# Optimization experiments

Hardware: AMD Instinct MI355X
Metric: run time of the kernel (lower is better)

The kernel has to match this reference:

```python
import jax, jax.numpy as jnp
import numpy as np

B, T, N, C, D = 8, 12, 1024, 64, 10

def setup_inputs() -> dict:
    key = jax.random.key(0)
    ks = jax.random.split(key, 7)
    x = jax.random.normal(ks[0], (B, T, N, C), dtype=jnp.float32)
    e1 = jax.random.normal(ks[1], (N, D), dtype=jnp.float32)
    e2 = jax.random.normal(ks[2], (N, D), dtype=jnp.float32)
    # buffer: sym-normalized adjacency after the __init__-time softmax
    A_sym = jax.random.uniform(ks[3], (N, N), dtype=jnp.float32)
    weights_pool = jax.random.normal(ks[4], (N, C, C), dtype=jnp.float32) * 0.02
    bias_pool = jax.random.normal(ks[5], (N, C), dtype=jnp.float32) * 0.02
    alpha = jnp.array([0.9], dtype=jnp.float32)
    beta = jnp.array([0.9], dtype=jnp.float32)
    gamma = jnp.array([0.1], dtype=jnp.float32)
    return {"x": x, "node_embeddings1": e1, "node_embeddings2": e2,
            "A_sym": A_sym, "weights_pool": weights_pool, "bias_pool": bias_pool,
            "alpha": alpha, "beta": beta, "gamma": gamma}


def reference(x, node_embeddings1, node_embeddings2, A_sym, weights_pool,
              bias_pool, alpha, beta, gamma):
    n = node_embeddings1.shape[0]
    # dynamic supports: relu(tanh(E1 E2^T - E2 E1^T)) + I
    s = jnp.tanh(node_embeddings1 @ node_embeddings2.T
                 - node_embeddings2 @ node_embeddings1.T)
    supports = jnp.eye(n, dtype=x.dtype) + jax.nn.relu(s)          # (N,N)

    # static branch: row-softmax of the precomputed sym-norm adjacency
    A = jax.nn.softmax(A_sym, axis=-1)                              # (N,N)
    x_static = jax.nn.relu(jnp.einsum('nm,btmc->btnc', A, x))       # (B,T,N,C)

    # spatial attention branch (note: softmax over the TIME axis, as in source)
    score = jnp.einsum('btnc,btmc->btnm', x, x)                     # (B,T,N,N)
    score = jax.nn.softmax(score, axis=1)
    x_sa = jax.nn.relu(jnp.einsum('btnm,btmc->btnc', score, x))     # (B,T,N,C)

    # adaptive graph conv: per-node weights/bias from supports
    weights = jnp.einsum('nd,dio->nio', supports, weights_pool)     # (N,C,C)
    bias = supports @ bias_pool                                     # (N,C)
    x_g = jnp.einsum('nm,btmc->btnc', supports, x)                  # (B,T,N,C)
    x_gconv = jax.nn.relu(jnp.einsum('btni,nio->btno', x_g, weights) + bias)

    return alpha * x_gconv + beta * x_sa + gamma * x_static
```

## Files before the change

kernel.cpp:

```cpp
#include <hip/hip_runtime.h>
#include <math.h>

#define Bdim 8
#define Tdim 12
#define BT   96
#define Ndim 1024
#define Cdim 64
#define Ddim 10
#define Jdim 6144
#define IOdim 4096

typedef __attribute__((ext_vector_type(4))) float f32x4;
typedef __attribute__((ext_vector_type(8))) short bf16x8;
typedef __attribute__((ext_vector_type(4))) _Float16 f16x4;

__device__ inline short f2bf(float f) {
    union { float f; unsigned u; } v; v.f = f;
    return (short)((v.u + 0x8000u) >> 16);
}
__device__ inline float bf2f(short s) {
    union { float f; unsigned u; } v; v.u = ((unsigned)(unsigned short)s) << 16;
    return v.f;
}
__device__ inline void load_lds16(const void* g, void* l) {
    __builtin_amdgcn_global_load_lds(
        (const __attribute__((address_space(1))) unsigned int*)g,
        (__attribute__((address_space(3))) unsigned int*)l, 16, 0, 0);
}
__device__ inline float fexp(float x) { return __expf(x); }
__device__ inline float frcp(float x) { return __builtin_amdgcn_rcpf(x); }
__device__ inline float flog(float x) { return __logf(x); }

__global__ __launch_bounds__(256) void k_supports(
    const float* __restrict__ e1, const float* __restrict__ e2,
    short* __restrict__ Sbf)
{
    int idx = blockIdx.x * 256 + threadIdx.x;
    int i = idx >> 10, j = idx & 1023;
    float s = 0.f;
#pragma unroll
    for (int d = 0; d < Ddim; ++d)
        s += e1[i * Ddim + d] * e2[j * Ddim + d]
           - e2[i * Ddim + d] * e1[j * Ddim + d];
    float t = 1.f - 2.f * frcp(fexp(2.f * s) + 1.f);
    float v = fmaxf(t, 0.f);
    if (i == j) v += 1.f;
    Sbf[idx] = f2bf(v);
}

__global__ __launch_bounds__(256) void k_softmax_rows(
    const float* __restrict__ In, short* __restrict__ Out)
{
    int row = blockIdx.x;
    const float* r = In + (size_t)row * Ndim;
    short* o = Out + (size_t)row * Ndim;
    __shared__ float red[256];
    int tid = threadIdx.x;
    float vals[4];
    float lmax = -INFINITY;
#pragma unroll
    for (int i = 0; i < 4; ++i) { vals[i] = r[tid + 256 * i]; lmax = fmaxf(lmax, vals[i]); }
    red[tid] = lmax; __syncthreads();
    for (int s = 128; s > 0; s >>= 1) {
        if (tid < s) red[tid] = fmaxf(red[tid], red[tid + s]);
        __syncthreads();
    }
    float m = red[0]; __syncthreads();
    float lsum = 0.f;
#pragma unroll
    for (int i = 0; i < 4; ++i) { vals[i] = fexp(vals[i] - m); lsum += vals[i]; }
    red[tid] = lsum; __syncthreads();
    for (int s = 128; s > 0; s >>= 1) {
        if (tid < s) red[tid] += red[tid + s];
        __syncthreads();
    }
    float inv = frcp(red[0]);
#pragma unroll
    for (int i = 0; i < 4; ++i) o[tid + 256 * i] = f2bf(vals[i] * inv);
}

__global__ __launch_bounds__(256) void k_cvt_x(
    const float* __restrict__ x, short* __restrict__ xbf, short* __restrict__ xT)
{
    __shared__ float Lt[64][65];
    int bt = blockIdx.y, n0 = blockIdx.x * 64;
    const float* src = x + (size_t)bt * 65536 + (size_t)n0 * 64;
    int tid = threadIdx.x;
#pragma unroll
    for (int p = 0; p < 4; ++p) {
        int idx = p * 256 + tid;
        int r = idx >> 4, c4 = idx & 15;
        float4 v = *(const float4*)&src[r * 64 + c4 * 4];
        short4 s4 = make_short4(f2bf(v.x), f2bf(v.y), f2bf(v.z), f2bf(v.w));
        *(short4*)&xbf[(size_t)bt * 65536 + (size_t)(n0 + r) * 64 + c4 * 4] = s4;
        Lt[r][c4 * 4 + 0] = v.x; Lt[r][c4 * 4 + 1] = v.y;
        Lt[r][c4 * 4 + 2] = v.z; Lt[r][c4 * 4 + 3] = v.w;
    }
    __syncthreads();
#pragma unroll
    for (int p = 0; p < 4; ++p) {
        int idx = p * 256 + tid;
        int c = idx >> 4, k4 = idx & 15;
        short4 s4 = make_short4(f2bf(Lt[k4 * 4 + 0][c]), f2bf(Lt[k4 * 4 + 1][c]),
                                f2bf(Lt[k4 * 4 + 2][c]), f2bf(Lt[k4 * 4 + 3][c]));
        *(short4*)&xT[(size_t)bt * 65536 + (size_t)c * 1024 + n0 + k4 * 4] = s4;
    }
}

__global__ __launch_bounds__(256) void k_cvt_wp(
    const float* __restrict__ wp, short* __restrict__ wpT)
{
    __shared__ float Lt[64][65];
    int k0 = blockIdx.y * 64, j0 = blockIdx.x * 64;
    int tid = threadIdx.x;
#pragma unroll
    for (int p = 0; p < 4; ++p) {
        int idx = p * 256 + tid;
        int r = idx >> 4, c4 = idx & 15;
        float4 v = *(const float4*)&wp[(size_t)(k0 + r) * IOdim + j0 + c4 * 4];
        Lt[r][c4 * 4 + 0] = v.x; Lt[r][c4 * 4 + 1] = v.y;
        Lt[r][c4 * 4 + 2] = v.z; Lt[r][c4 * 4 + 3] = v.w;
    }
    __syncthreads();
#pragma unroll
    for (int p = 0; p < 4; ++p) {
        int idx = p * 256 + tid;
        int c = idx >> 4, k4 = idx & 15;
        short4 s4 = make_short4(f2bf(Lt[k4 * 4 + 0][c]), f2bf(Lt[k4 * 4 + 1][c]),
                                f2bf(Lt[k4 * 4 + 2][c]), f2bf(Lt[k4 * 4 + 3][c]));
        *(short4*)&wpT[(size_t)(j0 + c) * 1024 + k0 + k4 * 4] = s4;
    }
}

__global__ __launch_bounds__(256) void k_cvt_bp(
    const float* __restrict__ bp, short* __restrict__ bpT)
{
    __shared__ float Lt[64][65];
    int k0 = blockIdx.x * 64;
    int tid = threadIdx.x;
#pragma unroll
    for (int p = 0; p < 4; ++p) {
        int idx = p * 256 + tid;
        int r = idx >> 4, c4 = idx & 15;
        float4 v = *(const float4*)&bp[(size_t)(k0 + r) * 64 + c4 * 4];
        Lt[r][c4 * 4 + 0] = v.x; Lt[r][c4 * 4 + 1] = v.y;
        Lt[r][c4 * 4 + 2] = v.z; Lt[r][c4 * 4 + 3] = v.w;
    }
    __syncthreads();
#pragma unroll
    for (int p = 0; p < 4; ++p) {
        int idx = p * 256 + tid;
        int c = idx >> 4, k4 = idx & 15;
        short4 s4 = make_short4(f2bf(Lt[k4 * 4 + 0][c]), f2bf(Lt[k4 * 4 + 1][c]),
                                f2bf(Lt[k4 * 4 + 2][c]), f2bf(Lt[k4 * 4 + 3][c]));
        *(short4*)&bpT[(size_t)c * 1024 + k0 + k4 * 4] = s4;
    }
}

template<int MODE>
__global__ __launch_bounds__(256) void k_gemm_bt(
    const short* __restrict__ A, const short* __restrict__ Bm,
    float* __restrict__ Cf, short* __restrict__ Cb,
    const float* __restrict__ gamma_p)
{
    __shared__ short At[128 * 64];
    __shared__ short Bt[128 * 64];
    const int tid = threadIdx.x;
    const int w = tid >> 6, l = tid & 63;
    const int l15 = l & 15, q = l >> 4;
    const int n0 = blockIdx.x * 128, j0 = blockIdx.y * 128;
    const int wr = (w & 1) * 64, wc = (w >> 1) * 64;
    const int lrow = l >> 3, lc8 = l & 7;

    f32x4 acc[4][4];
#pragma unroll
    for (int i = 0; i < 4; ++i)
#pragma unroll
        for (int j = 0; j < 4; ++j) acc[i][j] = (f32x4)0.f;

    for (int k0 = 0; k0 < 1024; k0 += 64) {
        __syncthreads();
#pragma unroll
        for (int p = 0; p < 4; ++p) {
            int r = p * 32 + w * 8 + lrow;
            int sc = lc8 ^ (r & 7);
            load_lds16(A + (size_t)(n0 + r) * 1024 + k0 + sc * 8,
                       &At[(p * 32 + w * 8) * 64]);
            load_lds16(Bm + (size_t)(j0 + r) * 1024 + k0 + sc * 8,
                       &Bt[(p * 32 + w * 8) * 64]);
        }
        __syncthreads();
#pragma unroll
        for (int ks = 0; ks < 2; ++ks) {
            bf16x8 af[4], bf[4];
#pragma unroll
            for (int rt = 0; rt < 4; ++rt) {
                int row = wr + rt * 16 + l15;
                int pos = (ks * 4 + q) ^ (row & 7);
                af[rt] = *(const bf16x8*)&At[row * 64 + pos * 8];
            }
#pragma unroll
            for (int ct = 0; ct < 4; ++ct) {
                int row = wc + ct * 16 + l15;
                int pos = (ks * 4 + q) ^ (row & 7);
                bf[ct] = *(const bf16x8*)&Bt[row * 64 + pos * 8];
            }
#pragma unroll
            for (int rt = 0; rt < 4; ++rt)
#pragma unroll
                for (int ct = 0; ct < 4; ++ct)
                    acc[rt][ct] = __builtin_amdgcn_mfma_f32_16x16x32_bf16(
                        af[rt], bf[ct], acc[rt][ct], 0, 0, 0);
        }
    }

    float gmm = (MODE == 0) ? gamma_p[0] : 0.f;
#pragma unroll
    for (int rt = 0; rt < 4; ++rt) {
        int nr = n0 + wr + rt * 16 + q * 4;
#pragma unroll
        for (int ct = 0; ct < 4; ++ct) {
            int j = j0 + wc + ct * 16 + l15;
#pragma unroll
            for (int r = 0; r < 4; ++r) {
                float v = acc[rt][ct][r];
                int n = nr + r;
                if (MODE == 1) {
                    Cb[(size_t)n * IOdim + j] = f2bf(v);
                } else if (n < 1024) {
                    int bt = j >> 6, c = j & 63;
                    Cf[(size_t)bt * 65536 + (size_t)n * 64 + c] = gmm * fmaxf(v, 0.f);
                } else {
                    Cb[(size_t)(n - 1024) * Jdim + j] = f2bf(v);
                }
            }
        }
    }
}

__global__ __launch_bounds__(256, 4) void k_sa_z(
    const short* __restrict__ xbf, short* __restrict__ Lh)
{
    __shared__ short Xn[64 * 64];
    __shared__ short Xm[64 * 64];

    int id = blockIdx.x;
    int b = id & 7;
    int r = id >> 3;
    int tn = r & 15, tm = r >> 4;
    int tid = threadIdx.x;
    int w = tid >> 6, l = tid & 63;
    int l15 = l & 15, q = l >> 4;
    int lrow = l >> 3, lc8 = l & 7;
    int n0 = tn * 64, m0 = tm * 64;
    int wn = (w & 1) * 32, wm = (w >> 1) * 32;

    const short* Xb = xbf + (size_t)b * Tdim * Ndim * Cdim;
    short* Lb = Lh + ((size_t)b << 20);

    f32x4 M[2][2], Z[2][2];
#pragma unroll
    for (int nh = 0; nh < 2; ++nh)
#pragma unroll
        for (int mh = 0; mh < 2; ++mh) { M[nh][mh] = (f32x4)(-INFINITY); Z[nh][mh] = (f32x4)0.f; }

    for (int t = 0; t < Tdim; ++t) {
        const short* xt = Xb + (size_t)t * (Ndim * Cdim);
        __syncthreads();
#pragma unroll
        for (int p = 0; p < 2; ++p) {
            int rr = p * 32 + w * 8 + lrow;
            int sc = lc8 ^ (rr & 7);
            load_lds16(xt + (size_t)(n0 + rr) * 64 + sc * 8, &Xn[(p * 32 + w * 8) * 64]);
            load_lds16(xt + (size_t)(m0 + rr) * 64 + sc * 8, &Xm[(p * 32 + w * 8) * 64]);
        }
        __syncthreads();

        f32x4 sacc[2][2];
        sacc[0][0] = (f32x4)0.f; sacc[0][1] = (f32x4)0.f;
        sacc[1][0] = (f32x4)0.f; sacc[1][1] = (f32x4)0.f;
#pragma unroll
        for (int ch = 0; ch < 2; ++ch) {
            bf16x8 qb[2], af[2];
#pragma unroll
            for (int nh = 0; nh < 2; ++nh) {
                int row = wn + nh * 16 + l15;
                int pos = (ch * 4 + q) ^ (row & 7);
                qb[nh] = *(const bf16x8*)&Xn[row * 64 + pos * 8];
            }
#pragma unroll
            for (int mh = 0; mh < 2; ++mh) {
                int row = wm + mh * 16 + l15;
                int pos = (ch * 4 + q) ^ (row & 7);
                af[mh] = *(const bf16x8*)&Xm[row * 64 + pos * 8];
            }
#pragma unroll
            for (int nh = 0; nh < 2; ++nh)
#pragma unroll
                for (int mh = 0; mh < 2; ++mh)
                    sacc[nh][mh] = __builtin_amdgcn_mfma_f32_16x16x32_bf16(
                        af[mh], qb[nh], sacc[nh][mh], 0, 0, 0);
        }
#pragma unroll
        for (int nh = 0; nh < 2; ++nh)
#pragma unroll
            for (int mh = 0; mh < 2; ++mh)
#pragma unroll
                for (int i = 0; i < 4; ++i) {
                    float s  = sacc[nh][mh][i];
                    float mo = M[nh][mh][i];
                    float mn = fmaxf(mo, s);
                    Z[nh][mh][i] = Z[nh][mh][i] * fexp(mo - mn) + fexp(s - mn);
                    M[nh][mh][i] = mn;
                }
    }
#pragma unroll
    for (int nh = 0; nh < 2; ++nh)
#pragma unroll
        for (int mh = 0; mh < 2; ++mh) {
            f16x4 ev;
#pragma unroll
            for (int i = 0; i < 4; ++i)
                ev[i] = (_Float16)(M[nh][mh][i] + flog(Z[nh][mh][i]));
            *(f16x4*)&Lb[(size_t)(n0 + wn + nh * 16 + l15) * 1024
                         + m0 + wm + mh * 16 + q * 4] = ev;
        }
}

__global__ __launch_bounds__(256, 4) void k_sa_pv(
    const short* __restrict__ xbf, const short* __restrict__ xT,
    const short* __restrict__ Lh, float* __restrict__ Out,
    const float* __restrict__ beta_p)
{
    __shared__ short Xm[32 * 72];
    __shared__ short XTl[64 * 40];
    __shared__ short Pl[4][16][40];

    int id = blockIdx.x;
    int b = id & 7;
    int r = id >> 3;
    int nt = r & 7, t = r >> 3;
    int tid = threadIdx.x;
    int w = tid >> 6, l = tid & 63;
    int l15 = l & 15, q = l >> 4;
    int n0 = nt * 128 + w * 32;

    const short* Xb  = xbf + ((size_t)b * Tdim + t) * (Ndim * Cdim);
    const short* XTb = xT  + ((size_t)b * Tdim + t) * (Ndim * Cdim);
    const short* Lb  = Lh + ((size_t)b << 20);

    int srow  = tid >> 3, sc8 = tid & 7;
    int srow2 = tid >> 2, sc4 = tid & 3;

    bf16x8 qf[2][2];
#pragma unroll
    for (int nh = 0; nh < 2; ++nh)
#pragma unroll
        for (int ch = 0; ch < 2; ++ch)
            qf[nh][ch] = *(const bf16x8*)&Xb[(n0 + nh * 16 + l15) * 64 + ch * 32 + q * 8];

    f32x4 oacc[2][4];
#pragma unroll
    for (int nh = 0; nh < 2; ++nh)
#pragma unroll
        for (int ct = 0; ct < 4; ++ct) oacc[nh][ct] = (f32x4)0.f;

    bf16x8 v  = *(const bf16x8*)&Xb[(size_t)srow * 64 + sc8 * 8];
    bf16x8 v2 = *(const bf16x8*)&XTb[(size_t)srow2 * 1024 + sc4 * 8];
    f16x4 e[2][2];
#pragma unroll
    for (int nh = 0; nh < 2; ++nh)
#pragma unroll
        for (int mh = 0; mh < 2; ++mh)
            e[nh][mh] = *(const f16x4*)&Lb[(size_t)(n0 + nh * 16 + l15) * 1024
                                           + mh * 16 + q * 4];

    for (int mi = 0; mi < 32; ++mi) {
        __syncthreads();
        *(bf16x8*)&Xm[srow * 72 + sc8 * 8]   = v;
        *(bf16x8*)&XTl[srow2 * 40 + sc4 * 8] = v2;
        __syncthreads();

        int m0n = (mi < 31 ? mi + 1 : 31) * 32;
        bf16x8 vn  = *(const bf16x8*)&Xb[(size_t)(m0n + srow) * 64 + sc8 * 8];
        bf16x8 v2n = *(const bf16x8*)&XTb[(size_t)srow2 * 1024 + m0n + sc4 * 8];
        f16x4 en[2][2];
#pragma unroll
        for (int nh = 0; nh < 2; ++nh)
#pragma unroll
            for (int mh = 0; mh < 2; ++mh)
                en[nh][mh] = *(const f16x4*)&Lb[(size_t)(n0 + nh * 16 + l15) * 1024
                                                + m0n + mh * 16 + q * 4];

        f32x4 sacc[2][2];
        sacc[0][0] = (f32x4)0.f; sacc[0][1] = (f32x4)0.f;
        sacc[1][0] = (f32x4)0.f; sacc[1][1] = (f32x4)0.f;
#pragma unroll
        for (int ch = 0; ch < 2; ++ch) {
#pragma unroll
            for (int mh = 0; mh < 2; ++mh) {
                bf16x8 af = *(const bf16x8*)&Xm[(mh * 16 + l15) * 72 + ch * 32 + q * 8];
                sacc[0][mh] = __builtin_amdgcn_mfma_f32_16x16x32_bf16(
                    af, qf[0][ch], sacc[0][mh], 0, 0, 0);
                sacc[1][mh] = __builtin_amdgcn_mfma_f32_16x16x32_bf16(
                    af, qf[1][ch], sacc[1][mh], 0, 0, 0);
            }
        }
#pragma unroll
        for (int nh = 0; nh < 2; ++nh) {
#pragma unroll
            for (int mh = 0; mh < 2; ++mh) {
                f32x4 p = sacc[nh][mh];
                f16x4 ee = e[nh][mh];
                unsigned u0 = (unsigned)(unsigned short)f2bf(fexp(p[0] - (float)ee[0]))
                            | ((unsigned)(unsigned short)f2bf(fexp(p[1] - (float)ee[1])) << 16);
                unsigned u1 = (unsigned)(unsigned short)f2bf(fexp(p[2] - (float)ee[2]))
                            | ((unsigned)(unsigned short)f2bf(fexp(p[3] - (float)ee[3])) << 16);
                *(uint2*)&Pl[w][l15][mh * 16 + q * 4] = make_uint2(u0, u1);
            }
            bf16x8 pf = *(const bf16x8*)&Pl[w][l15][q * 8];
#pragma unroll
            for (int ct = 0; ct < 4; ++ct) {
                bf16x8 bfr = *(const bf16x8*)&XTl[(ct * 16 + l15) * 40 + q * 8];
                oacc[nh][ct] = __builtin_amdgcn_mfma_f32_16x16x32_bf16(
                    pf, bfr, oacc[nh][ct], 0, 0, 0);
            }
        }
        v = vn; v2 = v2n;
#pragma unroll
        for (int nh = 0; nh < 2; ++nh)
#pragma unroll
            for (int mh = 0; mh < 2; ++mh) e[nh][mh] = en[nh][mh];
    }

    float beta = beta_p[0];
#pragma unroll
    for (int nh = 0; nh < 2; ++nh)
#pragma unroll
        for (int ct = 0; ct < 4; ++ct)
#pragma unroll
            for (int r2 = 0; r2 < 4; ++r2) {
                size_t idx = (((size_t)b * Tdim + t) * Ndim + n0 + nh * 16 + q * 4 + r2) * Cdim
                           + ct * 16 + l15;
                Out[idx] += beta * fmaxf(oacc[nh][ct][r2], 0.f);
            }
}

__global__ __launch_bounds__(256) void k_bias(
    const short* __restrict__ Sbf, const short* __restrict__ bpT,
    float* __restrict__ bias)
{
    int tid = threadIdx.x;
    int w = tid >> 6, l = tid & 63;
    int l15 = l & 15, q = l >> 4;
    int nr = blockIdx.x * 64 + w * 16;

    f32x4 acc[4];
#pragma unroll
    for (int ct = 0; ct < 4; ++ct) acc[ct] = (f32x4)0.f;

    for (int k0 = 0; k0 < 1024; k0 += 32) {
        bf16x8 af = *(const bf16x8*)&Sbf[(size_t)(nr + l15) * 1024 + k0 + q * 8];
#pragma unroll
        for (int ct = 0; ct < 4; ++ct) {
            bf16x8 bf = *(const bf16x8*)&bpT[(size_t)(ct * 16 + l15) * 1024 + k0 + q * 8];
            acc[ct] = __builtin_amdgcn_mfma_f32_16x16x32_bf16(af, bf, acc[ct], 0, 0, 0);
        }
    }
#pragma unroll
    for (int ct = 0; ct < 4; ++ct)
#pragma unroll
        for (int r = 0; r < 4; ++r)
            bias[(size_t)(nr + q * 4 + r) * 64 + ct * 16 + l15] = acc[ct][r];
}

__global__ __launch_bounds__(384) void k_gconv(
    const short* __restrict__ xgT, const short* __restrict__ Wb,
    const float* __restrict__ bias, float* __restrict__ Out,
    const float* __restrict__ alpha_p)
{
    __shared__ short Wl[64 * 64];
    int n = blockIdx.x;
    int tid = threadIdx.x;
    for (int f = tid; f < 512; f += 384) {
        int k = f >> 3, j = f & 7;
        *(bf16x8*)&Wl[k * 64 + (j ^ ((k >> 3) & 7)) * 8] =
            *(const bf16x8*)&Wb[(size_t)n * IOdim + f * 8];
    }
    __syncthreads();
    int w = tid / 64, l = tid & 63, l15 = l & 15, q = l >> 4;
    f32x4 acc[4];
#pragma unroll
    for (int ct = 0; ct < 4; ++ct) acc[ct] = (f32x4)0.f;
    const short* xr = xgT + (size_t)n * Jdim + (size_t)(w * 16 + l15) * 64;
#pragma unroll
    for (int ks = 0; ks < 2; ++ks) {
        bf16x8 a = *(const bf16x8*)&xr[ks * 32 + q * 8];
        int kb = ks * 32 + q * 8;
        int msk = (kb >> 3) & 7;
#pragma unroll
        for (int ct = 0; ct < 4; ++ct) {
            bf16x8 bfr;
#pragma unroll
            for (int e = 0; e < 8; ++e) {
                int o = ct * 16 + l15;
                bfr[e] = Wl[(kb + e) * 64 + (((o >> 3) ^ msk) * 8) + (o & 7)];
            }
            acc[ct] = __builtin_amdgcn_mfma_f32_16x16x32_bf16(a, bfr, acc[ct], 0, 0, 0);
        }
    }
    float alpha = alpha_p[0];
#pragma unroll
    for (int ct = 0; ct < 4; ++ct) {
        int o = ct * 16 + l15;
        float bo = bias[(size_t)n * 64 + o];
#pragma unroll
        for (int r = 0; r < 4; ++r) {
            int bt = w * 16 + q * 4 + r;
            size_t idx = (size_t)bt * 65536 + (size_t)n * 64 + o;
            Out[idx] += alpha * fmaxf(acc[ct][r] + bo, 0.f);
        }
    }
}

extern "C" void kernel_launch(void* const* d_in, const int* in_sizes, int n_in,
                              void* d_out, int out_size, void* d_ws, size_t ws_size,
                              hipStream_t stream)
{
    const float* x     = (const float*)d_in[0];
    const float* e1    = (const float*)d_in[1];
    const float* e2    = (const float*)d_in[2];
    const float* Asym  = (const float*)d_in[3];
    const float* wpool = (const float*)d_in[4];
    const float* bpool = (const float*)d_in[5];
    const float* alpha = (const float*)d_in[6];
    const float* beta  = (const float*)d_in[7];
    const float* gamma = (const float*)d_in[8];
    float* out = (float*)d_out;

    short* ASbf = (short*)d_ws;
    short* xbf  = ASbf + 2048 * 1024;
    short* xT   = xbf  + 6291456;
    short* wpT  = xT   + 6291456;
    short* Wbf  = wpT  + 4194304;
    short* xgT  = Wbf  + 4194304;
    float* bias = (float*)(xgT + 6291456);
    short* Lh   = (short*)(bias + 65536);
    short* bpT  = Lh + 8388608;

    k_supports<<<4096, 256, 0, stream>>>(e1, e2, ASbf + 1024 * 1024);
    k_softmax_rows<<<1024, 256, 0, stream>>>(Asym, ASbf);
    k_cvt_x<<<dim3(16, 96), 256, 0, stream>>>(x, xbf, xT);
    k_cvt_wp<<<dim3(64, 16), 256, 0, stream>>>(wpool, wpT);
    k_cvt_bp<<<16, 256, 0, stream>>>(bpool, bpT);
    k_sa_z<<<2048, 256, 0, stream>>>(xbf, Lh);
    k_gemm_bt<0><<<dim3(16, 48), 256, 0, stream>>>(ASbf, xT, out, xgT, gamma);
    k_gemm_bt<1><<<dim3(8, 32), 256, 0, stream>>>(ASbf + 1024 * 1024, wpT, nullptr, Wbf, nullptr);
    k_bias<<<16, 256, 0, stream>>>(ASbf + 1024 * 1024, bpT, bias);
    k_sa_pv<<<768, 256, 0, stream>>>(xbf, xT, Lh, out, beta);
    k_gconv<<<1024, 384, 0, stream>>>(xgT, Wbf, bias, out, alpha);
}
```

Baseline: 322.0 us.

## Double-buffer LDS tiles and widen key tile to 64 in attention PV kernel

The spatial-attention PV kernel now processes 64 keys per iteration instead of 32 and keeps two LDS buffers for the X and X-transpose tiles. This halves the iteration count and drops to a single barrier per iteration, cutting synchronisation overhead and letting the global prefetch of the next tile overlap compute. In exchange LDS use and register pressure grow, and the occupancy hint falls from 4 to 3 blocks per CU. The log-sum-exp loads are no longer prefetched one iteration ahead.

```diff
diff --git a/kernel.cpp b/kernel.cpp
--- a/kernel.cpp
+++ b/kernel.cpp
@@ -327,14 +327,14 @@
         }
 }
 
-__global__ __launch_bounds__(256, 4) void k_sa_pv(
+__global__ __launch_bounds__(256, 3) void k_sa_pv(
     const short* __restrict__ xbf, const short* __restrict__ xT,
     const short* __restrict__ Lh, float* __restrict__ Out,
     const float* __restrict__ beta_p)
 {
-    __shared__ short Xm[32 * 72];
-    __shared__ short XTl[64 * 40];
-    __shared__ short Pl[4][16][40];
+    __shared__ short Xm[2][64 * 72];
+    __shared__ short XTl[2][64 * 72];
+    __shared__ short Pl[4][16][72];
 
     int id = blockIdx.x;
     int b = id & 7;
@@ -349,8 +349,7 @@
     const short* XTb = xT  + ((size_t)b * Tdim + t) * (Ndim * Cdim);
     const short* Lb  = Lh + ((size_t)b << 20);
 
-    int srow  = tid >> 3, sc8 = tid & 7;
-    int srow2 = tid >> 2, sc4 = tid & 3;
+    int srow = tid >> 2, sc4 = tid & 3;
 
     bf16x8 qf[2][2];
 #pragma unroll
@@ -365,41 +364,46 @@
 #pragma unroll
         for (int ct = 0; ct < 4; ++ct) oacc[nh][ct] = (f32x4)0.f;
 
-    bf16x8 v  = *(const bf16x8*)&Xb[(size_t)srow * 64 + sc8 * 8];
-    bf16x8 v2 = *(const bf16x8*)&XTb[(size_t)srow2 * 1024 + sc4 * 8];
-    f16x4 e[2][2];
-#pragma unroll
-    for (int nh = 0; nh < 2; ++nh)
-#pragma unroll
-        for (int mh = 0; mh < 2; ++mh)
-            e[nh][mh] = *(const f16x4*)&Lb[(size_t)(n0 + nh * 16 + l15) * 1024
-                                           + mh * 16 + q * 4];
-
-    for (int mi = 0; mi < 32; ++mi) {
-        __syncthreads();
-        *(bf16x8*)&Xm[srow * 72 + sc8 * 8]   = v;
-        *(bf16x8*)&XTl[srow2 * 40 + sc4 * 8] = v2;
-        __syncthreads();
-
-        int m0n = (mi < 31 ? mi + 1 : 31) * 32;
-        bf16x8 vn  = *(const bf16x8*)&Xb[(size_t)(m0n + srow) * 64 + sc8 * 8];
-        bf16x8 v2n = *(const bf16x8*)&XTb[(size_t)srow2 * 1024 + m0n + sc4 * 8];
-        f16x4 en[2][2];
+    bf16x8 v[2], v2[2];
+#pragma unroll
+    for (int p = 0; p < 2; ++p) {
+        v[p]  = *(const bf16x8*)&Xb[(size_t)srow * 64 + (sc4 + 4 * p) * 8];
+        v2[p] = *(const bf16x8*)&XTb[(size_t)srow * 1024 + (sc4 + 4 * p) * 8];
+    }
+
+    for (int mi = 0; mi < 16; ++mi) {
+        int cur = mi & 1;
+        int m0 = mi * 64;
+#pragma unroll
+        for (int p = 0; p < 2; ++p) {
+            *(bf16x8*)&Xm[cur][srow * 72 + (sc4 + 4 * p) * 8]  = v[p];
+            *(bf16x8*)&XTl[cur][srow * 72 + (sc4 + 4 * p) * 8] = v2[p];
+        }
+        int m0n = (mi < 15) ? m0 + 64 : m0;
+#pragma unroll
+        for (int p = 0; p < 2; ++p) {
+            v[p]  = *(const bf16x8*)&Xb[(size_t)(m0n + srow) * 64 + (sc4 + 4 * p) * 8];
+            v2[p] = *(const bf16x8*)&XTb[(size_t)srow * 1024 + m0n + (sc4 + 4 * p) * 8];
+        }
+        f16x4 e[2][4];
 #pragma unroll
         for (int nh = 0; nh < 2; ++nh)
 #pragma unroll
-            for (int mh = 0; mh < 2; ++mh)
-                en[nh][mh] = *(const f16x4*)&Lb[(size_t)(n0 + nh * 16 + l15) * 1024
-                                                + m0n + mh * 16 + q * 4];
-
-        f32x4 sacc[2][2];
-        sacc[0][0] = (f32x4)0.f; sacc[0][1] = (f32x4)0.f;
-        sacc[1][0] = (f32x4)0.f; sacc[1][1] = (f32x4)0.f;
+            for (int mh = 0; mh < 4; ++mh)
+                e[nh][mh] = *(const f16x4*)&Lb[(size_t)(n0 + nh * 16 + l15) * 1024
+                                               + m0 + mh * 16 + q * 4];
+        __syncthreads();
+
+        f32x4 sacc[2][4];
+#pragma unroll
+        for (int nh = 0; nh < 2; ++nh)
+#pragma unroll
+            for (int mh = 0; mh < 4; ++mh) sacc[nh][mh] = (f32x4)0.f;
 #pragma unroll
         for (int ch = 0; ch < 2; ++ch) {
 #pragma unroll
-            for (int mh = 0; mh < 2; ++mh) {
-                bf16x8 af = *(const bf16x8*)&Xm[(mh * 16 + l15) * 72 + ch * 32 + q * 8];
+            for (int mh = 0; mh < 4; ++mh) {
+                bf16x8 af = *(const bf16x8*)&Xm[cur][(mh * 16 + l15) * 72 + ch * 32 + q * 8];
                 sacc[0][mh] = __builtin_amdgcn_mfma_f32_16x16x32_bf16(
                     af, qf[0][ch], sacc[0][mh], 0, 0, 0);
                 sacc[1][mh] = __builtin_amdgcn_mfma_f32_16x16x32_bf16(
@@ -409,7 +413,7 @@
 #pragma unroll
         for (int nh = 0; nh < 2; ++nh) {
 #pragma unroll
-            for (int mh = 0; mh < 2; ++mh) {
+            for (int mh = 0; mh < 4; ++mh) {
                 f32x4 p = sacc[nh][mh];
                 f16x4 ee = e[nh][mh];
                 unsigned u0 = (unsigned)(unsigned short)f2bf(fexp(p[0] - (float)ee[0]))
@@ -418,19 +422,17 @@
                             | ((unsigned)(unsigned short)f2bf(fexp(p[3] - (float)ee[3])) << 16);
                 *(uint2*)&Pl[w][l15][mh * 16 + q * 4] = make_uint2(u0, u1);
             }
-            bf16x8 pf = *(const bf16x8*)&Pl[w][l15][q * 8];
-#pragma unroll
-            for (int ct = 0; ct < 4; ++ct) {
-                bf16x8 bfr = *(const bf16x8*)&XTl[(ct * 16 + l15) * 40 + q * 8];
-                oacc[nh][ct] = __builtin_amdgcn_mfma_f32_16x16x32_bf16(
-                    pf, bfr, oacc[nh][ct], 0, 0, 0);
-            }
-        }
-        v = vn; v2 = v2n;
-#pragma unroll
-        for (int nh = 0; nh < 2; ++nh)
-#pragma unroll
-            for (int mh = 0; mh < 2; ++mh) e[nh][mh] = en[nh][mh];
+#pragma unroll
+            for (int ks = 0; ks < 2; ++ks) {
+                bf16x8 pf = *(const bf16x8*)&Pl[w][l15][ks * 32 + q * 8];
+#pragma unroll
+                for (int ct = 0; ct < 4; ++ct) {
+                    bf16x8 bfr = *(const bf16x8*)&XTl[cur][(ct * 16 + l15) * 72 + ks * 32 + q * 8];
+                    oacc[nh][ct] = __builtin_amdgcn_mfma_f32_16x16x32_bf16(
+                        pf, bfr, oacc[nh][ct], 0, 0, 0);
+                }
+            }
+        }
     }
 
     float beta = beta_p[0];
```

Measured after the change: 322.3 us. No clear change (+0.1%).
